# Performance work log

Measured on AMD Instinct MI355X. Metric: run time of the kernel, lower is better.

## Reference

```python
import jax, jax.numpy as jnp
import numpy as np

THETA = 10000.0
B, S, D, H = 2, 2048, 1024, 16
DK = D // H


def setup_inputs() -> dict:
    key = jax.random.key(0)
    k1, k2, k3 = jax.random.split(key, 3)
    x = jax.random.normal(k1, (B, S, D), jnp.float32)
    # trunc_normal init approximated by scaled normal (std = 2/(d_k+d_model))
    weight = jax.random.normal(k2, (3, H, DK, D), jnp.float32) * (2.0 / (DK + D))
    wo_weight = jax.random.normal(k3, (D, H * DK), jnp.float32) * (2.0 / (2 * D))
    token_positions = jnp.arange(S, dtype=jnp.int32)
    return {"x": x, "token_positions": token_positions, "weight": weight, "wo_weight": wo_weight}


def _rope(x, cos, sin):
    # x: (..., seq, d_k); rotate interleaved pairs
    x1 = jnp.stack((-x[..., 1::2], x[..., ::2]), axis=-1).reshape(x.shape)
    return x * cos + x1 * sin


def _masked_softmax(scores, mask):
    # matches reference: exp(x - rowmax over ALL entries), zero masked, normalize, zero again
    e = jnp.exp(scores - jnp.max(scores, axis=-1, keepdims=True))
    e = jnp.where(mask, e, 0.0)
    a = e / jnp.sum(e, axis=-1, keepdims=True)
    return jnp.where(mask, a, 0.0)


def reference(x, token_positions, weight, wo_weight):
    dk = weight.shape[2]
    seq_len = x.shape[-2]
    # fused QKV projection: (b, 3, h, s, dk)
    qkv = jnp.einsum('bsd,qhkd->bqhsk', x, weight)
    # RoPE tables from token positions
    pos = token_positions.astype(jnp.float32)[:, None]          # (s, 1)
    kidx = jnp.arange(1, dk // 2 + 1, dtype=jnp.float32)[None]  # (1, dk/2)
    theta = pos / (THETA ** ((2.0 * kidx - 2.0) / dk))          # (s, dk/2)
    cos = jnp.repeat(jnp.cos(theta), 2, axis=-1)                # (s, dk)
    sin = jnp.repeat(jnp.sin(theta), 2, axis=-1)
    q = _rope(qkv[:, 0], cos, sin)   # (b, h, s, dk)
    k = _rope(qkv[:, 1], cos, sin)
    v = qkv[:, 2]
    scores = jnp.einsum('bhqd,bhkd->bhqk', q, k) / jnp.sqrt(jnp.float32(dk))
    mask = jnp.tril(jnp.ones((seq_len, seq_len), dtype=bool))
    att = _masked_softmax(scores, mask)
    out = jnp.einsum('bhqk,bhkd->bhqd', att, v)                 # (b, h, s, dv)
    out = jnp.transpose(out, (0, 2, 1, 3)).reshape(*x.shape[:-1], -1)  # (b, s, h*dv)
    return jnp.einsum('bsi,oi->bso', out, wo_weight)
```

## Files before the change

kernel.cpp:

```cpp
#include <hip/hip_runtime.h>
#include <hip/hip_bf16.h>
#include <math.h>

#define B_   2
#define S_   2048
#define D_   1024
#define H_   16
#define DK_  64
#define NQKV 3072
#define M_   (B_ * S_)

typedef unsigned short u16;
typedef unsigned int   u32;
typedef __attribute__((ext_vector_type(8))) short short8;
typedef __attribute__((ext_vector_type(4))) float f32x4;
typedef __attribute__((ext_vector_type(4))) u16   u16x4;

typedef const __attribute__((address_space(1))) void* gvptr;
typedef __attribute__((address_space(3))) void* lvptr;

#define QSCALE 0.18033688011f

#if __has_builtin(__builtin_amdgcn_exp2f)
#define EXP2F(x) __builtin_amdgcn_exp2f(x)
#else
#define EXP2F(x) __expf(0.69314718056f * (x))
#endif

__device__ __forceinline__ u16 f2bf(float f) {
  union { float f; u32 u; } v; v.f = f;
  u32 r = v.u + 0x7FFF + ((v.u >> 16) & 1);
  return (u16)(r >> 16);
}
__device__ __forceinline__ float bf2f(u16 h) {
  union { u32 u; float f; } v; v.u = ((u32)h) << 16;
  return v.f;
}
__device__ __forceinline__ u32 cvtpk_bf16(float lo, float hi) {
  u32 r;
  asm("v_cvt_pk_bf16_f32 %0, %1, %2" : "=v"(r) : "v"(lo), "v"(hi));
  return r;
}

#define MEMFENCE() asm volatile("" ::: "memory")
#define RAW_BARRIER() do { MEMFENCE(); __builtin_amdgcn_s_barrier(); MEMFENCE(); } while (0)

#define SWZ(r) ((((r) & 7) ^ ((((r) >> 3) & 1) << 2)))

#define N4X (M_ * D_ / 4)
#define N4W (NQKV * D_ / 4)
#define N4WO (D_ * D_ / 4)
#define NCVT (N4X + N4W + N4WO)
__global__ void cvt_all_kernel(const float* __restrict__ x,
                               const float* __restrict__ w,
                               const float* __restrict__ wo,
                               u16* __restrict__ dst,
                               const int* __restrict__ pos,
                               float2* __restrict__ cs) {
  int i = blockIdx.x * 256 + threadIdx.x;
  if (i < NCVT) {
    float4 v;
    if (i < N4X)            v = ((const float4*)x)[i];
    else if (i < N4X + N4W) v = ((const float4*)w)[i - N4X];
    else                    v = ((const float4*)wo)[i - (N4X + N4W)];
    u16x4 o;
    o[0] = f2bf(v.x); o[1] = f2bf(v.y); o[2] = f2bf(v.z); o[3] = f2bf(v.w);
    ((u16x4*)dst)[i] = o;
  } else {
    int idx = i - NCVT;
    int fi = idx & 31;
    int s = idx >> 5;
    double p = (double)pos[s];
    double t = p * pow(10000.0, -(double)fi / 32.0);
    cs[idx] = make_float2((float)cos(t), (float)sin(t));
  }
}

__global__ __launch_bounds__(256) void gemm_qkv_mfma(const u16* __restrict__ A,
                                                     const u16* __restrict__ Bm,
                                                     u16* __restrict__ qkvb,
                                                     u16* __restrict__ Vt,
                                                     const float2* __restrict__ cstab) {
  __shared__ u16 lds[2 * 128 * 64];
  u16* Asp = lds;
  u16* Bsp = lds + 128 * 64;
  const int t  = threadIdx.x;
  const int w  = t >> 6, l = t & 63;
  const int g  = l >> 4, ln = l & 15;
  const int wm = w >> 1, wn = w & 1;
  const int m0 = blockIdx.y * 128, n0 = blockIdx.x * 128;
  const int Kd = D_, Nd = NQKV;

  const f32x4 vzero = {0.f, 0.f, 0.f, 0.f};
  f32x4 acc[4][4];
#pragma unroll
  for (int i = 0; i < 4; ++i)
#pragma unroll
    for (int j = 0; j < 4; ++j) acc[i][j] = vzero;

  for (int k0 = 0; k0 < Kd; k0 += 64) {
    __syncthreads();
#pragma unroll
    for (int p = 0; p < 4; ++p) {
      int c = p * 256 + t;
      int r = c >> 3, sx = (c & 7) ^ (r & 7);
      __builtin_amdgcn_global_load_lds(
          (gvptr)(A + (size_t)(m0 + r) * Kd + k0 + sx * 8),
          (lvptr)(&Asp[(p * 256 + w * 64) * 8]), 16, 0, 0);
      __builtin_amdgcn_global_load_lds(
          (gvptr)(Bm + (size_t)(n0 + r) * Kd + k0 + sx * 8),
          (lvptr)(&Bsp[(p * 256 + w * 64) * 8]), 16, 0, 0);
    }
    __syncthreads();

#pragma unroll
    for (int ks = 0; ks < 2; ++ks) {
      short8 af[4], bf[4];
#pragma unroll
      for (int i = 0; i < 4; ++i) {
        int ra = wm * 64 + i * 16 + ln;
        af[i] = *(const short8*)&Asp[ra * 64 + (((ks * 4 + g) ^ (ra & 7)) * 8)];
        int rb = wn * 64 + i * 16 + ln;
        bf[i] = *(const short8*)&Bsp[rb * 64 + (((ks * 4 + g) ^ (rb & 7)) * 8)];
      }
#pragma unroll
      for (int i = 0; i < 4; ++i)
#pragma unroll
        for (int j = 0; j < 4; ++j)
          acc[i][j] = __builtin_amdgcn_mfma_f32_16x16x32_bf16(af[i], bf[j], acc[i][j], 0, 0, 0);
    }
  }

  if (n0 < 2048) {
#pragma unroll
    for (int i = 0; i < 4; ++i)
#pragma unroll
      for (int r = 0; r < 4; ++r) {
        int rowi = m0 + wm * 64 + i * 16 + g * 4 + r;
        int srow = rowi & (S_ - 1);
#pragma unroll
        for (int j = 0; j < 4; ++j) {
          int dk = j * 16 + ln;
          float2 cs = cstab[srow * 32 + (dk >> 1)];
          float v = acc[i][j][r];
          float p = __shfl_xor(v, 1);
          float sn = (ln & 1) ? cs.y : -cs.y;
          float rot = fmaf(p, sn, v * cs.x);
          qkvb[(size_t)rowi * Nd + n0 + wn * 64 + j * 16 + ln] = f2bf(rot);
        }
      }
  } else {
    __syncthreads();
    u16* tr = lds;
#pragma unroll
    for (int i = 0; i < 4; ++i)
#pragma unroll
      for (int j = 0; j < 4; ++j) {
        int col = wn * 64 + j * 16 + ln;
        int rowb = wm * 64 + i * 16 + g * 4;
#pragma unroll
        for (int r = 0; r < 4; ++r)
          tr[col * 128 + ((rowb + r) ^ ((col & 7) << 3))] = f2bf(acc[i][j][r]);
      }
    __syncthreads();
    {
      int col = t >> 1, half = t & 1;
      int hh = ((n0 - 2048) >> 6) + (col >> 6);
      int dk = col & 63;
      int bb = m0 >> 11, sb = m0 & 2047;
      u16* dstp = Vt + ((size_t)(bb * H_ + hh) * 64 + dk) * S_ + sb + half * 64;
      const u16* srcp = tr + col * 128 + half * 64;
      int p7 = col & 7;
#pragma unroll
      for (int q = 0; q < 8; ++q)
        *(uint4*)(dstp + q * 8) = *(const uint4*)(srcp + ((q ^ p7) * 8));
    }
  }
}

__global__ __launch_bounds__(256) void gemm_small_mfma(const u16* __restrict__ A,
                                                       const u16* __restrict__ Bm,
                                                       float* __restrict__ C,
                                                       int Nd, int Kd) {
  __shared__ u16 As[2][64 * 64];
  __shared__ u16 Bs[2][64 * 64];
  const int t  = threadIdx.x;
  const int w  = t >> 6, l = t & 63;
  const int g  = l >> 4, ln = l & 15;
  const int wm = w >> 1, wn = w & 1;
  const int m0 = blockIdx.y * 64, n0 = blockIdx.x * 64;

  auto stage = [&](int buf, int k0) {
#pragma unroll
    for (int p = 0; p < 2; ++p) {
      int c = p * 256 + t;
      int r = c >> 3;
      int sx = (c & 7) ^ (r & 7);
      __builtin_amdgcn_global_load_lds(
          (gvptr)(A + (size_t)(m0 + r) * Kd + k0 + sx * 8),
          (lvptr)(&As[buf][(p * 256 + w * 64) * 8]), 16, 0, 0);
      __builtin_amdgcn_global_load_lds(
          (gvptr)(Bm + (size_t)(n0 + r) * Kd + k0 + sx * 8),
          (lvptr)(&Bs[buf][(p * 256 + w * 64) * 8]), 16, 0, 0);
    }
  };

  const f32x4 vzero = {0.f, 0.f, 0.f, 0.f};
  f32x4 acc[2][2];
#pragma unroll
  for (int i = 0; i < 2; ++i)
#pragma unroll
    for (int j = 0; j < 2; ++j) acc[i][j] = vzero;

  const int nkt = Kd >> 6;
  stage(0, 0);
  int cur = 0;
#pragma unroll 1
  for (int kt = 0; kt < nkt; ++kt) {
    if (kt + 1 < nkt) {
      stage(cur ^ 1, (kt + 1) * 64);
      asm volatile("s_waitcnt vmcnt(4)" ::: "memory");
    } else {
      asm volatile("s_waitcnt vmcnt(0)" ::: "memory");
    }
    RAW_BARRIER();

    __builtin_amdgcn_s_setprio(1);
#pragma unroll
    for (int ks = 0; ks < 2; ++ks) {
      short8 af[2], bf[2];
#pragma unroll
      for (int i = 0; i < 2; ++i) {
        int ra = wm * 32 + i * 16 + ln;
        af[i] = *(const short8*)&As[cur][ra * 64 + (((ks * 4 + g) ^ (ra & 7)) * 8)];
        int rb = wn * 32 + i * 16 + ln;
        bf[i] = *(const short8*)&Bs[cur][rb * 64 + (((ks * 4 + g) ^ (rb & 7)) * 8)];
      }
#pragma unroll
      for (int i = 0; i < 2; ++i)
#pragma unroll
        for (int j = 0; j < 2; ++j)
          acc[i][j] = __builtin_amdgcn_mfma_f32_16x16x32_bf16(af[i], bf[j], acc[i][j], 0, 0, 0);
    }
    __builtin_amdgcn_s_setprio(0);

    asm volatile("s_waitcnt lgkmcnt(0)" ::: "memory");
    RAW_BARRIER();
    cur ^= 1;
  }

#pragma unroll
  for (int i = 0; i < 2; ++i)
#pragma unroll
    for (int j = 0; j < 2; ++j)
#pragma unroll
      for (int r = 0; r < 4; ++r)
        C[(size_t)(m0 + wm * 32 + i * 16 + g * 4 + r) * Nd + n0 + wn * 32 + j * 16 + ln]
            = acc[i][j][r];
}

__global__ __launch_bounds__(512) void attn_mfma(const u16* __restrict__ qkvb,
                                                 const u16* __restrict__ Vt,
                                                 u16* __restrict__ attb) {
  __shared__ u16 Ks[2][128 * 64];
  __shared__ u16 Vs[2][64 * 128];
  const int t = threadIdx.x;
  const int w = t >> 6, l = t & 63;
  const int g = l >> 4, ln = l & 15;
  const int id = blockIdx.x;
  const int xcd = id & 7, slot = id >> 3;
  const int pair = xcd * 4 + (slot & 3);
  const int bx = slot >> 2;
  const int b = pair >> 4, h = pair & 15;
  const size_t bS = (size_t)b * S_;
  const u16* Kbase = qkvb + bS * NQKV + D_ + h * 64;
  const u16* Vbase = Vt + (size_t)(b * H_ + h) * 64 * S_;

  auto stage = [&](int buf, int k0) {
#pragma unroll
    for (int p = 0; p < 2; ++p) {
      int ck = p * 512 + t;
      int rk = ck >> 3, sk = (ck & 7) ^ SWZ(rk);
      __builtin_amdgcn_global_load_lds(
          (gvptr)(Kbase + (size_t)(k0 + rk) * NQKV + sk * 8),
          (lvptr)(&Ks[buf][(p * 512 + w * 64) * 8]), 16, 0, 0);
      int cv = p * 512 + t;
      int rv = cv >> 4, sv = (cv & 15) ^ (rv & 15);
      __builtin_amdgcn_global_load_lds(
          (gvptr)(Vbase + (size_t)rv * S_ + k0 + sv * 8),
          (lvptr)(&Vs[buf][(p * 512 + w * 64) * 8]), 16, 0, 0);
    }
  };

  const f32x4 vzero = {0.f, 0.f, 0.f, 0.f};

  const int tqH = 15 - bx, tqL = bx;
  const int q0H = tqH * 128, q0L = tqL * 128;
  const int nt = 16 - bx;
  const int ntL = bx + 1;
  const int qgH = q0H + w * 16 + ln;
  const int qgL = q0L + w * 16 + ln;

  short8 qfH[2], qfL[2];
  {
    const u16* qr = qkvb + (bS + q0H + w * 16 + ln) * NQKV + h * 64;
    qfH[0] = *(const short8*)(qr + g * 8);
    qfH[1] = *(const short8*)(qr + 32 + g * 8);
    qr = qkvb + (bS + q0L + w * 16 + ln) * NQKV + h * 64;
    qfL[0] = *(const short8*)(qr + g * 8);
    qfL[1] = *(const short8*)(qr + 32 + g * 8);
#pragma unroll
    for (int kx = 0; kx < 2; ++kx)
#pragma unroll
      for (int e = 0; e < 8; ++e) {
        qfH[kx][e] = (short)f2bf(bf2f((u16)qfH[kx][e]) * QSCALE);
        qfL[kx][e] = (short)f2bf(bf2f((u16)qfL[kx][e]) * QSCALE);
      }
  }

  f32x4 oH[4], oL[4];
#pragma unroll
  for (int dt = 0; dt < 4; ++dt) { oH[dt] = vzero; oL[dt] = vzero; }
  float mH = -INFINITY, lH = 0.f, mL = -INFINITY, lL = 0.f;

  auto chain = [&](const short8* qf, f32x4* o, float& mrun, float& lrun,
                   int qg, bool maskTile, int k0, int cur) {
    f32x4 sacc[8];
#pragma unroll
    for (int st = 0; st < 8; ++st) sacc[st] = vzero;
    __builtin_amdgcn_s_setprio(1);
#pragma unroll
    for (int st = 0; st < 8; ++st) {
      const int pr = ((ln >> 2) << 3) + ((st & 1) << 2) + (ln & 3) + ((st >> 1) << 5);
#pragma unroll
      for (int ks = 0; ks < 2; ++ks) {
        short8 kf = *(const short8*)&Ks[cur][pr * 64 + (((ks * 4 + g) ^ SWZ(pr)) * 8)];
        sacc[st] = __builtin_amdgcn_mfma_f32_16x16x32_bf16(kf, qf[ks], sacc[st], 0, 0, 0);
      }
    }
    __builtin_amdgcn_s_setprio(0);

    float tmax = -INFINITY;
    if (maskTile) {
#pragma unroll
      for (int st = 0; st < 8; ++st)
#pragma unroll
        for (int r = 0; r < 4; ++r) {
          int key = k0 + g * 8 + ((st & 1) << 2) + r + ((st >> 1) << 5);
          if (key > qg) sacc[st][r] = -INFINITY;
          tmax = fmaxf(tmax, sacc[st][r]);
        }
    } else {
#pragma unroll
      for (int st = 0; st < 8; ++st)
#pragma unroll
        for (int r = 0; r < 4; ++r) tmax = fmaxf(tmax, sacc[st][r]);
    }
    tmax = fmaxf(tmax, __shfl_xor(tmax, 16));
    tmax = fmaxf(tmax, __shfl_xor(tmax, 32));
    float al = 1.f, mnew = mrun;
    if (!__all(tmax <= mrun + 8.0f)) {
      mnew = fmaxf(mrun, tmax);
      al = EXP2F(mrun - mnew);
#pragma unroll
      for (int r = 0; r < 4; ++r) {
        float srs = __shfl(al, g * 4 + r);
#pragma unroll
        for (int dt = 0; dt < 4; ++dt) o[dt][r] *= srs;
      }
    }
    float lsum = 0.f;
#pragma unroll
    for (int st = 0; st < 8; ++st)
#pragma unroll
      for (int r = 0; r < 4; ++r) {
        float pe = EXP2F(sacc[st][r] - mnew);
        sacc[st][r] = pe;
        lsum += pe;
      }
    lsum += __shfl_xor(lsum, 16);
    lsum += __shfl_xor(lsum, 32);
    lrun = lrun * al + lsum;
    mrun = mnew;

    union { u32 u[4]; short8 v; } pa[4];
#pragma unroll
    for (int ks = 0; ks < 4; ++ks) {
      pa[ks].u[0] = cvtpk_bf16(sacc[2 * ks][0], sacc[2 * ks][1]);
      pa[ks].u[1] = cvtpk_bf16(sacc[2 * ks][2], sacc[2 * ks][3]);
      pa[ks].u[2] = cvtpk_bf16(sacc[2 * ks + 1][0], sacc[2 * ks + 1][1]);
      pa[ks].u[3] = cvtpk_bf16(sacc[2 * ks + 1][2], sacc[2 * ks + 1][3]);
    }

    __builtin_amdgcn_s_setprio(1);
#pragma unroll
    for (int ks = 0; ks < 4; ++ks)
#pragma unroll
      for (int dt = 0; dt < 4; ++dt) {
        const int dr = dt * 16 + ln;
        short8 vf = *(const short8*)&Vs[cur][dr * 128 + (((ks * 4 + g) ^ (dr & 15)) * 8)];
        o[dt] = __builtin_amdgcn_mfma_f32_16x16x32_bf16(pa[ks].v, vf, o[dt], 0, 0, 0);
      }
    __builtin_amdgcn_s_setprio(0);
  };

  stage(0, 0);
  int cur = 0;
#pragma unroll 1
  for (int kt = 0; kt < nt; ++kt) {
    const int k0 = kt * 128;
    if (kt + 1 < nt) {
      stage(cur ^ 1, k0 + 128);
      asm volatile("s_waitcnt vmcnt(4)" ::: "memory");
    } else {
      asm volatile("s_waitcnt vmcnt(0)" ::: "memory");
    }
    RAW_BARRIER();

    chain(qfH, oH, mH, lH, qgH, kt == nt - 1, k0, cur);
    if (kt < ntL)
      chain(qfL, oL, mL, lL, qgL, kt == tqL, k0, cur);

    asm volatile("s_waitcnt lgkmcnt(0)" ::: "memory");
    RAW_BARRIER();
    cur ^= 1;
  }

  {
    float linv = 1.f / lH;
#pragma unroll
    for (int r = 0; r < 4; ++r) {
      float ir = __shfl(linv, g * 4 + r);
      size_t row = bS + q0H + w * 16 + g * 4 + r;
#pragma unroll
      for (int dt = 0; dt < 4; ++dt)
        attb[row * D_ + h * 64 + dt * 16 + ln] = f2bf(oH[dt][r] * ir);
    }
  }
  {
    float linv = 1.f / lL;
#pragma unroll
    for (int r = 0; r < 4; ++r) {
      float ir = __shfl(linv, g * 4 + r);
      size_t row = bS + q0L + w * 16 + g * 4 + r;
#pragma unroll
      for (int dt = 0; dt < 4; ++dt)
        attb[row * D_ + h * 64 + dt * 16 + ln] = f2bf(oL[dt][r] * ir);
    }
  }
}

extern "C" void kernel_launch(void* const* d_in, const int* in_sizes, int n_in,
                              void* d_out, int out_size, void* d_ws, size_t ws_size,
                              hipStream_t stream) {
  (void)in_sizes; (void)n_in; (void)out_size; (void)ws_size;
  const float* x   = (const float*)d_in[0];
  const int*   pos = (const int*)d_in[1];
  const float* w   = (const float*)d_in[2];
  const float* wo  = (const float*)d_in[3];
  float* out = (float*)d_out;

  u16* qkvb = (u16*)d_ws;
  u16* Vt   = qkvb + (size_t)M_ * NQKV;
  u16* attb = Vt + (size_t)B_ * H_ * 64 * S_;
  u16* xb   = attb + (size_t)M_ * D_;
  u16* wb   = xb + (size_t)M_ * D_;
  u16* wob  = wb + (size_t)NQKV * D_;
  float2* cstab = (float2*)(wob + (size_t)D_ * D_);

  cvt_all_kernel<<<NCVT / 256 + 256, 256, 0, stream>>>(x, w, wo, xb, pos, cstab);

  gemm_qkv_mfma<<<dim3(NQKV / 128, M_ / 128), 256, 0, stream>>>(
      xb, wb, qkvb, Vt, cstab);

  attn_mfma<<<dim3(256), 512, 0, stream>>>(qkvb, Vt, attb);

  gemm_small_mfma<<<dim3(D_ / 64, M_ / 64), 256, 0, stream>>>(
      attb, wob, out, D_, D_);
}
```

Before: 185.7 us.

## Enlarge QKV GEMM tiles to 256x256 with double-buffered LDS and XCD-aware mapping

The QKV projection GEMM moves from 128x128 tiles with 256 threads to 256x256 tiles with 512 threads. Global-to-LDS loads are double buffered so the next K slice streams in while MFMAs run on the current one. Blocks are remapped onto a 1D grid so that neighbouring tiles land on the same XCD for L2 reuse, and the V-transpose epilogue is adapted to the larger tile. The cost is heavier register pressure (8x4 accumulators) and 128 KB of LDS per block, and the 192-block grid may leave some CUs idle.

After: 178.5 us. 1.04x faster.

```diff
diff --git a/kernel.cpp b/kernel.cpp
--- a/kernel.cpp
+++ b/kernel.cpp
@@ -76,67 +76,93 @@
   }
 }
 
-__global__ __launch_bounds__(256) void gemm_qkv_mfma(const u16* __restrict__ A,
+__global__ __launch_bounds__(512) void gemm_qkv_mfma(const u16* __restrict__ A,
                                                      const u16* __restrict__ Bm,
                                                      u16* __restrict__ qkvb,
                                                      u16* __restrict__ Vt,
                                                      const float2* __restrict__ cstab) {
-  __shared__ u16 lds[2 * 128 * 64];
-  u16* Asp = lds;
-  u16* Bsp = lds + 128 * 64;
+  __shared__ u16 lds[65536];
   const int t  = threadIdx.x;
   const int w  = t >> 6, l = t & 63;
   const int g  = l >> 4, ln = l & 15;
-  const int wm = w >> 1, wn = w & 1;
-  const int m0 = blockIdx.y * 128, n0 = blockIdx.x * 128;
+  const int wm = w >> 2, wn = w & 3;
+  const int id = blockIdx.x;
+  const int xcd = id & 7, s_ = id >> 3;
+  const int by = (xcd >> 1) * 4 + (s_ & 3);
+  const int bx = (xcd & 1) * 6 + (s_ >> 2);
+  const int m0 = by * 256, n0 = bx * 256;
   const int Kd = D_, Nd = NQKV;
 
-  const f32x4 vzero = {0.f, 0.f, 0.f, 0.f};
-  f32x4 acc[4][4];
-#pragma unroll
-  for (int i = 0; i < 4; ++i)
-#pragma unroll
-    for (int j = 0; j < 4; ++j) acc[i][j] = vzero;
-
-  for (int k0 = 0; k0 < Kd; k0 += 64) {
-    __syncthreads();
+  auto As = [&](int slot) { return lds + slot * 32768; };
+  auto Bs = [&](int slot) { return lds + slot * 32768 + 16384; };
+
+  auto stage = [&](int slot, int k0) {
 #pragma unroll
     for (int p = 0; p < 4; ++p) {
-      int c = p * 256 + t;
+      int c = p * 512 + t;
       int r = c >> 3, sx = (c & 7) ^ (r & 7);
       __builtin_amdgcn_global_load_lds(
           (gvptr)(A + (size_t)(m0 + r) * Kd + k0 + sx * 8),
-          (lvptr)(&Asp[(p * 256 + w * 64) * 8]), 16, 0, 0);
+          (lvptr)(&As(slot)[(p * 512 + w * 64) * 8]), 16, 0, 0);
       __builtin_amdgcn_global_load_lds(
           (gvptr)(Bm + (size_t)(n0 + r) * Kd + k0 + sx * 8),
-          (lvptr)(&Bsp[(p * 256 + w * 64) * 8]), 16, 0, 0);
-    }
-    __syncthreads();
-
+          (lvptr)(&Bs(slot)[(p * 512 + w * 64) * 8]), 16, 0, 0);
+    }
+  };
+
+  const f32x4 vzero = {0.f, 0.f, 0.f, 0.f};
+  f32x4 acc[8][4];
+#pragma unroll
+  for (int i = 0; i < 8; ++i)
+#pragma unroll
+    for (int j = 0; j < 4; ++j) acc[i][j] = vzero;
+
+  const int nkt = Kd >> 6;
+  stage(0, 0);
+  int cur = 0;
+#pragma unroll 1
+  for (int kt = 0; kt < nkt; ++kt) {
+    if (kt + 1 < nkt) {
+      stage(cur ^ 1, (kt + 1) * 64);
+      asm volatile("s_waitcnt vmcnt(8)" ::: "memory");
+    } else {
+      asm volatile("s_waitcnt vmcnt(0)" ::: "memory");
+    }
+    RAW_BARRIER();
+
+    __builtin_amdgcn_s_setprio(1);
 #pragma unroll
     for (int ks = 0; ks < 2; ++ks) {
-      short8 af[4], bf[4];
-#pragma unroll
-      for (int i = 0; i < 4; ++i) {
-        int ra = wm * 64 + i * 16 + ln;
-        af[i] = *(const short8*)&Asp[ra * 64 + (((ks * 4 + g) ^ (ra & 7)) * 8)];
-        int rb = wn * 64 + i * 16 + ln;
-        bf[i] = *(const short8*)&Bsp[rb * 64 + (((ks * 4 + g) ^ (rb & 7)) * 8)];
-      }
-#pragma unroll
-      for (int i = 0; i < 4; ++i)
+      short8 af[8], bf[4];
+#pragma unroll
+      for (int i = 0; i < 8; ++i) {
+        int ra = wm * 128 + i * 16 + ln;
+        af[i] = *(const short8*)&As(cur)[ra * 64 + (((ks * 4 + g) ^ (ra & 7)) * 8)];
+      }
+#pragma unroll
+      for (int j = 0; j < 4; ++j) {
+        int rb = wn * 64 + j * 16 + ln;
+        bf[j] = *(const short8*)&Bs(cur)[rb * 64 + (((ks * 4 + g) ^ (rb & 7)) * 8)];
+      }
+#pragma unroll
+      for (int i = 0; i < 8; ++i)
 #pragma unroll
         for (int j = 0; j < 4; ++j)
           acc[i][j] = __builtin_amdgcn_mfma_f32_16x16x32_bf16(af[i], bf[j], acc[i][j], 0, 0, 0);
     }
+    __builtin_amdgcn_s_setprio(0);
+
+    asm volatile("s_waitcnt lgkmcnt(0)" ::: "memory");
+    RAW_BARRIER();
+    cur ^= 1;
   }
 
   if (n0 < 2048) {
 #pragma unroll
-    for (int i = 0; i < 4; ++i)
+    for (int i = 0; i < 8; ++i)
 #pragma unroll
       for (int r = 0; r < 4; ++r) {
-        int rowi = m0 + wm * 64 + i * 16 + g * 4 + r;
+        int rowi = m0 + wm * 128 + i * 16 + g * 4 + r;
         int srow = rowi & (S_ - 1);
 #pragma unroll
         for (int j = 0; j < 4; ++j) {
@@ -151,29 +177,29 @@
       }
   } else {
     __syncthreads();
-    u16* tr = lds;
-#pragma unroll
-    for (int i = 0; i < 4; ++i)
+#pragma unroll
+    for (int i = 0; i < 8; ++i)
 #pragma unroll
       for (int j = 0; j < 4; ++j) {
         int col = wn * 64 + j * 16 + ln;
-        int rowb = wm * 64 + i * 16 + g * 4;
+        int rowb = wm * 128 + i * 16 + g * 4;
+        int s8 = (col & 15) << 3;
 #pragma unroll
         for (int r = 0; r < 4; ++r)
-          tr[col * 128 + ((rowb + r) ^ ((col & 7) << 3))] = f2bf(acc[i][j][r]);
+          lds[col * 256 + ((rowb + r) ^ s8)] = f2bf(acc[i][j][r]);
       }
     __syncthreads();
     {
       int col = t >> 1, half = t & 1;
-      int hh = ((n0 - 2048) >> 6) + (col >> 6);
-      int dk = col & 63;
+      int vcol = (n0 - 2048) + col;
+      int hh = vcol >> 6, dk = vcol & 63;
       int bb = m0 >> 11, sb = m0 & 2047;
-      u16* dstp = Vt + ((size_t)(bb * H_ + hh) * 64 + dk) * S_ + sb + half * 64;
-      const u16* srcp = tr + col * 128 + half * 64;
-      int p7 = col & 7;
-#pragma unroll
-      for (int q = 0; q < 8; ++q)
-        *(uint4*)(dstp + q * 8) = *(const uint4*)(srcp + ((q ^ p7) * 8));
+      u16* dstp = Vt + ((size_t)(bb * H_ + hh) * 64 + dk) * S_ + sb + half * 128;
+      const u16* srcp = lds + col * 256;
+      int s8 = (col & 15) << 3;
+#pragma unroll
+      for (int q = 0; q < 16; ++q)
+        *(uint4*)(dstp + q * 8) = *(const uint4*)(srcp + (((half * 128 + q * 8) ^ s8)));
     }
   }
 }
@@ -470,8 +496,7 @@
 
   cvt_all_kernel<<<NCVT / 256 + 256, 256, 0, stream>>>(x, w, wo, xb, pos, cstab);
 
-  gemm_qkv_mfma<<<dim3(NQKV / 128, M_ / 128), 256, 0, stream>>>(
-      xb, wb, qkvb, Vt, cstab);
+  gemm_qkv_mfma<<<dim3(192), 512, 0, stream>>>(xb, wb, qkvb, Vt, cstab);
 
   attn_mfma<<<dim3(256), 512, 0, stream>>>(qkvb, Vt, attb);
 
```
